# Kernel optimization log

Measured on AMD Instinct MI355X. Metric: run time of the kernel, lower is better.

## Reference

```python
import jax, jax.numpy as jnp
import numpy as np

B, S, D = 4, 2048, 512
H = 8
HD = D // H  # 64


def setup_inputs() -> dict:
    key = jax.random.key(0)
    k1, k2, k3 = jax.random.split(key, 3)
    x = jax.random.normal(k1, (B, S, D), dtype=jnp.float32)
    w_qkv = jax.random.normal(k2, (3 * D, D), dtype=jnp.float32) * (D ** -0.5)
    w_out = jax.random.normal(k3, (D, D), dtype=jnp.float32) * (D ** -0.5)
    return {"x": x, "w_qkv": w_qkv, "w_out": w_out}


def reference(x, w_qkv, w_out):
    b, s, d = x.shape
    # qkv projection (no bias), split into q,k,v
    qkv = jnp.einsum('bsd,ed->bse', x, w_qkv)  # [b, s, 3*d]
    q, k, v = jnp.split(qkv, 3, axis=2)
    # [b, s, h*hd] -> [b, h, s, hd]
    def to_heads(t):
        return t.reshape(b, s, H, HD).transpose(0, 2, 1, 3)
    q, k, v = to_heads(q), to_heads(k), to_heads(v)
    # NOTE: original module only scales by sqrt(head_dim) when mask is given;
    # with mask=None softmax is over raw QK^T scores.
    scores = jnp.einsum('bnid,bnjd->bnij', q, k)  # [b, h, s, s]
    attn = jax.nn.softmax(scores, axis=-1)
    o = jnp.einsum('bnij,bnjd->bnid', attn, v)  # [b, h, s, hd]
    o = o.transpose(0, 2, 1, 3).reshape(b, s, d)
    # dropout is identity (eval / drop_prob=0)
    return jnp.einsum('bsd,ed->bse', o, w_out)
```

## Files before the change

kernel.cpp:

```cpp
#include <hip/hip_runtime.h>
#include <hip/hip_bf16.h>

constexpr int B_  = 4;
constexpr int S_  = 2048;
constexpr int D_  = 512;
constexpr int H_  = 8;
constexpr int HD_ = 64;
constexpr int M_  = B_ * S_;

constexpr float LOG2E = 1.4426950408889634f;

typedef __attribute__((ext_vector_type(8))) short short8v;
typedef __attribute__((ext_vector_type(8))) _Float16 half8v;
typedef __attribute__((ext_vector_type(8))) unsigned short ushort8v;
typedef __attribute__((ext_vector_type(4))) float float4v;
typedef __attribute__((ext_vector_type(16))) float float16v;

__device__ __forceinline__ unsigned short f2bf(float x) {
    unsigned u = __builtin_bit_cast(unsigned, x);
    u += 0x7fffu + ((u >> 16) & 1u);
    return (unsigned short)(u >> 16);
}
__device__ __forceinline__ float bf2f(unsigned short h) {
    return __builtin_bit_cast(float, ((unsigned)h) << 16);
}
__device__ __forceinline__ unsigned short f2h(float x) {
    return __builtin_bit_cast(unsigned short, (_Float16)x);
}
__device__ __forceinline__ float fast_exp2(float x) {
#if __has_builtin(__builtin_amdgcn_exp2f)
    return __builtin_amdgcn_exp2f(x);
#else
    return exp2f(x);
#endif
}
__device__ __forceinline__ unsigned pack_bf16_trunc(float lo, float hi) {
    const unsigned ulo = __builtin_bit_cast(unsigned, lo);
    const unsigned uhi = __builtin_bit_cast(unsigned, hi);
#if __has_builtin(__builtin_amdgcn_perm)
    return __builtin_amdgcn_perm(uhi, ulo, 0x07060302u);
#else
    return (uhi & 0xffff0000u) | (ulo >> 16);
#endif
}
__device__ __forceinline__ void gload_lds16(const void* g, void* lds) {
    __builtin_amdgcn_global_load_lds((const __attribute__((address_space(1))) unsigned*)g,
                                     (__attribute__((address_space(3))) unsigned*)lds, 16, 0, 0);
}

__global__ __launch_bounds__(256) void prepass(const float* __restrict__ x,
                                               const float* __restrict__ wqkv,
                                               const float* __restrict__ wout,
                                               unsigned short* __restrict__ Xp,
                                               unsigned short* __restrict__ Wh,
                                               unsigned short* __restrict__ Wlq,
                                               unsigned short* __restrict__ Wob) {
    const int bid = blockIdx.x, t = threadIdx.x;
    if (bid < 2048) {
        const int flat = bid * 256 + t;
        const int m = flat >> 6, c = (flat & 63) * 8;
        const float4 a = *(const float4*)&x[(size_t)m * 512 + c];
        const float4 b = *(const float4*)&x[(size_t)m * 512 + c + 4];
        const float v[8] = {a.x, a.y, a.z, a.w, b.x, b.y, b.z, b.w};
        ushort8v hi, lo;
#pragma unroll
        for (int i = 0; i < 8; ++i) {
            const unsigned short h = f2bf(v[i]);
            hi[i] = h; lo[i] = f2bf(v[i] - bf2f(h));
        }
        *(ushort8v*)&Xp[(size_t)m * 1024 + c]       = hi;
        *(ushort8v*)&Xp[(size_t)m * 1024 + 512 + c] = lo;
    } else if (bid < 2048 + 384) {
        const int flat = (bid - 2048) * 256 + t;
        const int e = flat >> 6, c = (flat & 63) * 8;
        const float4 a = *(const float4*)&wqkv[(size_t)e * 512 + c];
        const float4 b = *(const float4*)&wqkv[(size_t)e * 512 + c + 4];
        const float v[8] = {a.x, a.y, a.z, a.w, b.x, b.y, b.z, b.w};
        ushort8v hi, lo;
#pragma unroll
        for (int i = 0; i < 8; ++i) {
            const unsigned short h = f2bf(v[i]);
            hi[i] = h; lo[i] = f2bf(v[i] - bf2f(h));
        }
        *(ushort8v*)&Wh[(size_t)e * 512 + c] = hi;
        if (e < 512) *(ushort8v*)&Wlq[(size_t)e * 512 + c] = lo;
    } else {
        const int flat = (bid - 2432) * 256 + t;
        const int e = flat >> 6, c = (flat & 63) * 8;
        const float4 a = *(const float4*)&wout[(size_t)e * 512 + c];
        const float4 b = *(const float4*)&wout[(size_t)e * 512 + c + 4];
        const float v[8] = {a.x, a.y, a.z, a.w, b.x, b.y, b.z, b.w};
        ushort8v hi;
#pragma unroll
        for (int i = 0; i < 8; ++i) hi[i] = f2bf(v[i]);
        *(ushort8v*)&Wob[(size_t)e * 512 + c] = hi;
    }
}

__global__ __launch_bounds__(256, 2) void gemm_qkv(const unsigned short* __restrict__ Xp,
                                                   const unsigned short* __restrict__ Wh,
                                                   const unsigned short* __restrict__ Wlq,
                                                   unsigned short* __restrict__ Qf,
                                                   unsigned short* __restrict__ KH,
                                                   unsigned short* __restrict__ VT) {
    __shared__ unsigned short Asm[2][128 * 64];
    __shared__ unsigned short Bsm[2][128 * 64];
    const int t = threadIdx.x, wv = t >> 6, lane = t & 63;
    const int fm = lane & 15, fq = lane >> 4;
    const int bid0 = blockIdx.x + 12 * blockIdx.y;
    const int xcd = bid0 & 7, ii = bid0 >> 3;
    const int x  = ii % 12;
    const int m0 = ((ii / 12) * 8 + xcd) * 128;
    const int slice = x >> 2;
    const int e0 = (x & 3) * 128;
    const bool vblk = (slice == 2);
    const int kiters = (slice == 0) ? 24 : 8;
    const int wrow = (wv >> 1) * 64, wcol = (wv & 1) * 64;

    const unsigned short* BbaseWh =
        Wh + (size_t)(e0 + (slice == 1 ? 512 : (slice == 2 ? 1024 : 0))) * 512;
    const unsigned short* BbaseWlq = Wlq + (size_t)e0 * 512;

    const int srow = t >> 3;
    const int skb0 = t & 7;

    float4v acc[4][4];
#pragma unroll
    for (int i = 0; i < 4; ++i)
#pragma unroll
        for (int j = 0; j < 4; ++j) acc[i][j] = (float4v){0.f, 0.f, 0.f, 0.f};

    {
#pragma unroll
        for (int i = 0; i < 4; ++i) {
            const int row = srow + 32 * i;
            const int kb = skb0 ^ (row & 7);
            gload_lds16(Xp + (size_t)(m0 + row) * 1024 + kb * 8,
                        &Asm[0][(wv * 64 + 256 * i) * 8]);
            gload_lds16(BbaseWh + (size_t)row * 512 + kb * 8,
                        &Bsm[0][(wv * 64 + 256 * i) * 8]);
        }
    }

    for (int kk = 0; kk < kiters; ++kk) {
        __syncthreads();

        if (kk + 1 < kiters) {
            const int nk = kk + 1;
            const int pass = nk >> 3;
            const int k0n = (nk & 7) * 64;
            const int nbuf = nk & 1;
            const int aoff = (slice == 0 && pass == 1) ? 512 : 0;
            const unsigned short* Bp = (slice == 0 && pass == 2) ? BbaseWlq : BbaseWh;
#pragma unroll
            for (int i = 0; i < 4; ++i) {
                const int row = srow + 32 * i;
                const int kb = skb0 ^ (row & 7);
                gload_lds16(Xp + (size_t)(m0 + row) * 1024 + aoff + k0n + kb * 8,
                            &Asm[nbuf][(wv * 64 + 256 * i) * 8]);
                gload_lds16(Bp + (size_t)row * 512 + k0n + kb * 8,
                            &Bsm[nbuf][(wv * 64 + 256 * i) * 8]);
            }
        }

        const int buf = kk & 1;
#pragma unroll
        for (int ks = 0; ks < 2; ++ks) {
            short8v af[4], bf[4];
#pragma unroll
            for (int mt = 0; mt < 4; ++mt) {
                const int row = wrow + mt * 16 + fm;
                af[mt] = *(const short8v*)&Asm[buf][row * 64 + 8 * ((4 * ks + fq) ^ (row & 7))];
            }
#pragma unroll
            for (int nt = 0; nt < 4; ++nt) {
                const int row = wcol + nt * 16 + fm;
                bf[nt] = *(const short8v*)&Bsm[buf][row * 64 + 8 * ((4 * ks + fq) ^ (row & 7))];
            }
            if (vblk) {
#pragma unroll
                for (int mt = 0; mt < 4; ++mt)
#pragma unroll
                    for (int nt = 0; nt < 4; ++nt)
                        acc[mt][nt] = __builtin_amdgcn_mfma_f32_16x16x32_bf16(bf[nt], af[mt], acc[mt][nt], 0, 0, 0);
            } else {
#pragma unroll
                for (int mt = 0; mt < 4; ++mt)
#pragma unroll
                    for (int nt = 0; nt < 4; ++nt)
                        acc[mt][nt] = __builtin_amdgcn_mfma_f32_16x16x32_bf16(af[mt], bf[nt], acc[mt][nt], 0, 0, 0);
            }
        }
    }

    if (!vblk) {
        unsigned short* __restrict__ dst = (slice == 0) ? Qf : KH;
        const float sc = (slice == 0) ? LOG2E : 1.0f;
#pragma unroll
        for (int mt = 0; mt < 4; ++mt)
#pragma unroll
            for (int nt = 0; nt < 4; ++nt) {
                const int e = e0 + wcol + nt * 16 + fm;
                const int h = e >> 6, hd = e & 63;
#pragma unroll
                for (int r = 0; r < 4; ++r) {
                    const int m = m0 + wrow + mt * 16 + 4 * fq + r;
                    const int b = m >> 11, s = m & 2047;
                    dst[((size_t)(b * 8 + h) * 2048 + s) * 64 + hd] =
                        f2h(acc[mt][nt][r] * sc);
                }
            }
    } else {
#pragma unroll
        for (int nt = 0; nt < 4; ++nt)
#pragma unroll
            for (int r = 0; r < 4; ++r) {
                const int e = e0 + wcol + nt * 16 + 4 * fq + r;
                const int h = e >> 6, hd = e & 63;
#pragma unroll
                for (int mt = 0; mt < 4; ++mt) {
                    const int m = m0 + wrow + mt * 16 + fm;
                    const int b = m >> 11, s = m & 2047;
                    const int s2 = (s & ~12) | ((s & 4) << 1) | ((s & 8) >> 1);
                    VT[((size_t)(b * 8 + h) * 64 + hd) * 2048 + s2] = f2bf(acc[mt][nt][r]);
                }
            }
    }
}

__global__ __launch_bounds__(256, 2) void attn(const unsigned short* __restrict__ Qfp,
                                               const unsigned short* __restrict__ KHp,
                                               const unsigned short* __restrict__ VTp,
                                               unsigned short* __restrict__ OB) {
    __shared__ unsigned short Ks[2][64 * 64];
    __shared__ unsigned short Vs[2][64 * 64];
    const int t = threadIdx.x, wv = t >> 6, lane = t & 63;
    const int lq = lane & 31;
    const int hf2 = lane >> 5;
    const int bid0 = blockIdx.x + 16 * blockIdx.y;
    const int xcd = bid0 & 7, ii = bid0 >> 3;
    const int bh = (ii & 3) * 8 + xcd;
    const int q0 = (ii >> 2) * 128;

    const unsigned short* qfp = Qfp + (size_t)bh * S_ * 64;
    const unsigned short* kh  = KHp + (size_t)bh * S_ * 64;
    const unsigned short* vt  = VTp + (size_t)bh * 64 * S_;

    const int srow = t >> 3;
    const int skb0 = t & 7;

#define STAGE_K(N, B) do {                                                      \
    _Pragma("unroll")                                                           \
    for (int i_ = 0; i_ < 2; ++i_) {                                            \
        const int row_ = srow + 32 * i_;                                        \
        const int kb_ = skb0 ^ (row_ & 7);                                      \
        gload_lds16(kh + (size_t)((N) * 64 + row_) * 64 + kb_ * 8,              \
                    &Ks[B][(wv * 64 + 256 * i_) * 8]);                          \
    } } while (0)

#define STAGE_V(N, B) do {                                                      \
    _Pragma("unroll")                                                           \
    for (int i_ = 0; i_ < 2; ++i_) {                                            \
        const int row_ = srow + 32 * i_;                                        \
        const int kb_ = skb0 ^ (row_ & 7);                                      \
        gload_lds16(vt + (size_t)row_ * S_ + (N) * 64 + kb_ * 8,                \
                    &Vs[B][(wv * 64 + 256 * i_) * 8]);                          \
    } } while (0)

#define QK_STEP(SN, KR) do {                                                    \
    _Pragma("unroll")                                                           \
    for (int jb_ = 0; jb_ < 2; ++jb_)                                           \
        _Pragma("unroll")                                                       \
        for (int r_ = 0; r_ < 16; ++r_) SN[jb_][r_] = 0.f;                      \
    _Pragma("unroll")                                                           \
    for (int kk_ = 0; kk_ < 4; ++kk_)                                           \
        _Pragma("unroll")                                                       \
        for (int jb_ = 0; jb_ < 2; ++jb_) {                                     \
            const int row_ = jb_ * 32 + lq;                                     \
            const int cb_ = 2 * kk_ + hf2;                                      \
            const half8v kf_ = *(const half8v*)&Ks[KR][row_ * 64 + 8 * (cb_ ^ (row_ & 7))]; \
            SN[jb_] = __builtin_amdgcn_mfma_f32_32x32x16_f16(kf_, qf[kk_], SN[jb_], 0, 0, 0); \
        } } while (0)

#define SOFTMAX_PV(SC, VR) do {                                                 \
    unsigned pk_[2][4][2];                                                      \
    _Pragma("unroll")                                                           \
    for (int jb_ = 0; jb_ < 2; ++jb_)                                           \
        _Pragma("unroll")                                                       \
        for (int g_ = 0; g_ < 4; ++g_) {                                        \
            const float p0_ = fast_exp2(SC[jb_][4 * g_ + 0]);                   \
            const float p1_ = fast_exp2(SC[jb_][4 * g_ + 1]);                   \
            const float p2_ = fast_exp2(SC[jb_][4 * g_ + 2]);                   \
            const float p3_ = fast_exp2(SC[jb_][4 * g_ + 3]);                   \
            lsum += (p0_ + p1_) + (p2_ + p3_);                                  \
            pk_[jb_][g_][0] = pack_bf16_trunc(p0_, p1_);                        \
            pk_[jb_][g_][1] = pack_bf16_trunc(p2_, p3_);                        \
        }                                                                       \
    __builtin_amdgcn_s_setprio(1);                                              \
    _Pragma("unroll")                                                           \
    for (int jc_ = 0; jc_ < 4; ++jc_) {                                         \
        const int jb_ = jc_ >> 1, gg_ = (jc_ & 1) * 2;                          \
        const uint4 uu_ = {pk_[jb_][gg_][0], pk_[jb_][gg_][1],                  \
                           pk_[jb_][gg_ + 1][0], pk_[jb_][gg_ + 1][1]};         \
        const short8v pa_ = __builtin_bit_cast(short8v, uu_);                   \
        _Pragma("unroll")                                                       \
        for (int db_ = 0; db_ < 2; ++db_) {                                     \
            const int vrow_ = db_ * 32 + lq;                                    \
            const int cb_ = 2 * jc_ + hf2;                                      \
            const short8v vf_ = *(const short8v*)&Vs[VR][vrow_ * 64 + 8 * (cb_ ^ (vrow_ & 7))]; \
            accO[db_] = __builtin_amdgcn_mfma_f32_32x32x16_bf16(pa_, vf_, accO[db_], 0, 0, 0);  \
        }                                                                       \
    }                                                                           \
    __builtin_amdgcn_s_setprio(0);                                              \
} while (0)

    STAGE_K(0, 0);
    STAGE_V(0, 0);
    STAGE_K(1, 1);

    half8v qf[4];
    {
        const int qrow = q0 + wv * 32 + lq;
#pragma unroll
        for (int kk = 0; kk < 4; ++kk)
            qf[kk] = *(const half8v*)&qfp[(size_t)qrow * 64 + kk * 16 + hf2 * 8];
    }

    float16v accO[2];
#pragma unroll
    for (int db = 0; db < 2; ++db)
#pragma unroll
        for (int r = 0; r < 16; ++r) accO[db][r] = 0.f;
    float lsum = 0.f;

    float16v sA[2], sB[2];

    __syncthreads();
    QK_STEP(sA, 0);
    __syncthreads();

    for (int jt = 0; jt < 32; jt += 2) {
        if (jt + 2 < 32) STAGE_K(jt + 2, 0);
        STAGE_V(jt + 1, 1);
        QK_STEP(sB, 1);
        SOFTMAX_PV(sA, 0);
        __syncthreads();
        if (jt + 3 < 32) STAGE_K(jt + 3, 1);
        if (jt + 2 < 32) {
            STAGE_V(jt + 2, 0);
            QK_STEP(sA, 0);
        }
        SOFTMAX_PV(sB, 1);
        __syncthreads();
    }

#undef STAGE_K
#undef STAGE_V
#undef QK_STEP
#undef SOFTMAX_PV

    const float ls = lsum + __shfl_xor(lsum, 32);
    const float invl = 1.f / ls;

    const int b = bh >> 3, hh = bh & 7;
#pragma unroll
    for (int g = 0; g < 4; ++g)
#pragma unroll
        for (int r = 0; r < 4; ++r) {
            const int qrow = r + 8 * g + 4 * hf2;
            const float inv = __shfl(invl, qrow);
            const int q = q0 + wv * 32 + qrow;
#pragma unroll
            for (int db = 0; db < 2; ++db)
                OB[((size_t)(b * 2048 + q)) * 512 + hh * 64 + db * 32 + lq] =
                    f2bf(accO[db][4 * g + r] * inv);
        }
}

__global__ __launch_bounds__(256) void gemm_out(const unsigned short* __restrict__ OB,
                                                const unsigned short* __restrict__ Wob,
                                                float* __restrict__ out) {
    __shared__ unsigned short Asm[2][128 * 64];
    __shared__ unsigned short Bsm[2][64 * 64];
    const int t = threadIdx.x, wv = t >> 6, lane = t & 63;
    const int fm = lane & 15, fq = lane >> 4;
    const int bid0 = blockIdx.x + 8 * blockIdx.y;
    const int xcd = bid0 & 7, ii = bid0 >> 3;
    const int e0 = (ii % 8) * 64;
    const int m0 = ((ii / 8) * 8 + xcd) * 128;
    const int wrow = (wv & 1) * 64, wcol = (wv >> 1) * 32;

    const int srow = t >> 3;
    const int skb0 = t & 7;

    float4v acc[4][2];
#pragma unroll
    for (int i = 0; i < 4; ++i)
#pragma unroll
        for (int j = 0; j < 2; ++j) acc[i][j] = (float4v){0.f, 0.f, 0.f, 0.f};

#pragma unroll
    for (int i = 0; i < 4; ++i) {
        const int row = srow + 32 * i;
        const int kb = skb0 ^ (row & 7);
        gload_lds16(OB + (size_t)(m0 + row) * 512 + kb * 8,
                    &Asm[0][(wv * 64 + 256 * i) * 8]);
    }
#pragma unroll
    for (int i = 0; i < 2; ++i) {
        const int row = srow + 32 * i;
        const int kb = skb0 ^ (row & 7);
        gload_lds16(Wob + (size_t)(e0 + row) * 512 + kb * 8,
                    &Bsm[0][(wv * 64 + 256 * i) * 8]);
    }

    for (int kk = 0; kk < 8; ++kk) {
        __syncthreads();
        if (kk + 1 < 8) {
            const int k0n = (kk + 1) * 64, nbuf = (kk + 1) & 1;
#pragma unroll
            for (int i = 0; i < 4; ++i) {
                const int row = srow + 32 * i;
                const int kb = skb0 ^ (row & 7);
                gload_lds16(OB + (size_t)(m0 + row) * 512 + k0n + kb * 8,
                            &Asm[nbuf][(wv * 64 + 256 * i) * 8]);
            }
#pragma unroll
            for (int i = 0; i < 2; ++i) {
                const int row = srow + 32 * i;
                const int kb = skb0 ^ (row & 7);
                gload_lds16(Wob + (size_t)(e0 + row) * 512 + k0n + kb * 8,
                            &Bsm[nbuf][(wv * 64 + 256 * i) * 8]);
            }
        }
        const int buf = kk & 1;
#pragma unroll
        for (int ks = 0; ks < 2; ++ks) {
            short8v af[4], bf[2];
#pragma unroll
            for (int mt = 0; mt < 4; ++mt) {
                const int row = wrow + mt * 16 + fm;
                af[mt] = *(const short8v*)&Asm[buf][row * 64 + 8 * ((4 * ks + fq) ^ (row & 7))];
            }
#pragma unroll
            for (int nt = 0; nt < 2; ++nt) {
                const int row = wcol + nt * 16 + fm;
                bf[nt] = *(const short8v*)&Bsm[buf][row * 64 + 8 * ((4 * ks + fq) ^ (row & 7))];
            }
#pragma unroll
            for (int mt = 0; mt < 4; ++mt)
#pragma unroll
                for (int nt = 0; nt < 2; ++nt)
                    acc[mt][nt] = __builtin_amdgcn_mfma_f32_16x16x32_bf16(af[mt], bf[nt], acc[mt][nt], 0, 0, 0);
        }
    }
#pragma unroll
    for (int mt = 0; mt < 4; ++mt)
#pragma unroll
        for (int nt = 0; nt < 2; ++nt)
#pragma unroll
            for (int r = 0; r < 4; ++r) {
                const int m = m0 + wrow + mt * 16 + 4 * fq + r;
                const int e = e0 + wcol + nt * 16 + fm;
                out[(size_t)m * 512 + e] = acc[mt][nt][r];
            }
}

extern "C" void kernel_launch(void* const* d_in, const int* in_sizes, int n_in,
                              void* d_out, int out_size, void* d_ws, size_t ws_size,
                              hipStream_t stream) {
    const float* x     = (const float*)d_in[0];
    const float* w_qkv = (const float*)d_in[1];
    const float* w_out = (const float*)d_in[2];
    float* out = (float*)d_out;

    char* p = (char*)d_ws;
    unsigned short* Xp  = (unsigned short*)p;  p += (size_t)M_ * 1024 * 2;
    unsigned short* Wh  = (unsigned short*)p;  p += (size_t)1536 * 512 * 2;
    unsigned short* Wlq = (unsigned short*)p;  p += (size_t)512 * 512 * 2;
    unsigned short* Wob = (unsigned short*)p;  p += (size_t)512 * 512 * 2;
    unsigned short* Qf  = (unsigned short*)p;  p += (size_t)32 * S_ * 64 * 2;
    unsigned short* KH  = (unsigned short*)p;  p += (size_t)32 * S_ * 64 * 2;
    unsigned short* VT  = (unsigned short*)p;  p += (size_t)32 * 64 * S_ * 2;
    unsigned short* OB  = Xp;

    prepass<<<2560, 256, 0, stream>>>(x, w_qkv, w_out, Xp, Wh, Wlq, Wob);
    gemm_qkv<<<dim3(12, 64), 256, 0, stream>>>(Xp, Wh, Wlq, Qf, KH, VT);
    attn<<<dim3(16, 32), 256, 0, stream>>>(Qf, KH, VT, OB);
    gemm_out<<<dim3(8, 64), 256, 0, stream>>>(OB, Wob, out);
}
```

Baseline: 161.1 us.

## Use single-pass fp16 QKV GEMM and enlarge output GEMM tiles

The QKV projection drops its split hi/lo bf16 scheme, where the Q slice ran three K passes. Inputs and weights are now converted once to fp16 and multiplied with f16 MFMA in a single pass, which cuts prepass writes and Q-slice GEMM work. The output GEMM moves from 128x64 to 128x128 tiles with 2-block occupancy to improve data reuse. The risk is lower Q precision feeding the unscaled softmax, and f2h must exist in the hidden helper lines.

```diff
diff --git a/kernel.cpp b/kernel.cpp
--- a/kernel.cpp
+++ b/kernel.cpp
@@ -51,9 +51,8 @@
 __global__ __launch_bounds__(256) void prepass(const float* __restrict__ x,
                                                const float* __restrict__ wqkv,
                                                const float* __restrict__ wout,
-                                               unsigned short* __restrict__ Xp,
-                                               unsigned short* __restrict__ Wh,
-                                               unsigned short* __restrict__ Wlq,
+                                               unsigned short* __restrict__ Xf,
+                                               unsigned short* __restrict__ Wf,
                                                unsigned short* __restrict__ Wob) {
     const int bid = blockIdx.x, t = threadIdx.x;
     if (bid < 2048) {
@@ -62,44 +61,35 @@
         const float4 a = *(const float4*)&x[(size_t)m * 512 + c];
         const float4 b = *(const float4*)&x[(size_t)m * 512 + c + 4];
         const float v[8] = {a.x, a.y, a.z, a.w, b.x, b.y, b.z, b.w};
-        ushort8v hi, lo;
-#pragma unroll
-        for (int i = 0; i < 8; ++i) {
-            const unsigned short h = f2bf(v[i]);
-            hi[i] = h; lo[i] = f2bf(v[i] - bf2f(h));
-        }
-        *(ushort8v*)&Xp[(size_t)m * 1024 + c]       = hi;
-        *(ushort8v*)&Xp[(size_t)m * 1024 + 512 + c] = lo;
+        ushort8v o;
+#pragma unroll
+        for (int i = 0; i < 8; ++i) o[i] = f2h(v[i]);
+        *(ushort8v*)&Xf[(size_t)m * 512 + c] = o;
     } else if (bid < 2048 + 384) {
         const int flat = (bid - 2048) * 256 + t;
         const int e = flat >> 6, c = (flat & 63) * 8;
         const float4 a = *(const float4*)&wqkv[(size_t)e * 512 + c];
         const float4 b = *(const float4*)&wqkv[(size_t)e * 512 + c + 4];
         const float v[8] = {a.x, a.y, a.z, a.w, b.x, b.y, b.z, b.w};
-        ushort8v hi, lo;
-#pragma unroll
-        for (int i = 0; i < 8; ++i) {
-            const unsigned short h = f2bf(v[i]);
-            hi[i] = h; lo[i] = f2bf(v[i] - bf2f(h));
-        }
-        *(ushort8v*)&Wh[(size_t)e * 512 + c] = hi;
-        if (e < 512) *(ushort8v*)&Wlq[(size_t)e * 512 + c] = lo;
+        ushort8v o;
+#pragma unroll
+        for (int i = 0; i < 8; ++i) o[i] = f2h(v[i]);
+        *(ushort8v*)&Wf[(size_t)e * 512 + c] = o;
     } else {
         const int flat = (bid - 2432) * 256 + t;
         const int e = flat >> 6, c = (flat & 63) * 8;
         const float4 a = *(const float4*)&wout[(size_t)e * 512 + c];
         const float4 b = *(const float4*)&wout[(size_t)e * 512 + c + 4];
         const float v[8] = {a.x, a.y, a.z, a.w, b.x, b.y, b.z, b.w};
-        ushort8v hi;
-#pragma unroll
-        for (int i = 0; i < 8; ++i) hi[i] = f2bf(v[i]);
-        *(ushort8v*)&Wob[(size_t)e * 512 + c] = hi;
-    }
-}
-
-__global__ __launch_bounds__(256, 2) void gemm_qkv(const unsigned short* __restrict__ Xp,
-                                                   const unsigned short* __restrict__ Wh,
-                                                   const unsigned short* __restrict__ Wlq,
+        ushort8v o;
+#pragma unroll
+        for (int i = 0; i < 8; ++i) o[i] = f2bf(v[i]);
+        *(ushort8v*)&Wob[(size_t)e * 512 + c] = o;
+    }
+}
+
+__global__ __launch_bounds__(256, 2) void gemm_qkv(const unsigned short* __restrict__ Xf,
+                                                   const unsigned short* __restrict__ Wf,
                                                    unsigned short* __restrict__ Qf,
                                                    unsigned short* __restrict__ KH,
                                                    unsigned short* __restrict__ VT) {
@@ -114,12 +104,9 @@
     const int slice = x >> 2;
     const int e0 = (x & 3) * 128;
     const bool vblk = (slice == 2);
-    const int kiters = (slice == 0) ? 24 : 8;
     const int wrow = (wv >> 1) * 64, wcol = (wv & 1) * 64;
 
-    const unsigned short* BbaseWh =
-        Wh + (size_t)(e0 + (slice == 1 ? 512 : (slice == 2 ? 1024 : 0))) * 512;
-    const unsigned short* BbaseWlq = Wlq + (size_t)e0 * 512;
+    const unsigned short* Bbase = Wf + (size_t)(e0 + slice * 512) * 512;
 
     const int srow = t >> 3;
     const int skb0 = t & 7;
@@ -130,35 +117,29 @@
 #pragma unroll
         for (int j = 0; j < 4; ++j) acc[i][j] = (float4v){0.f, 0.f, 0.f, 0.f};
 
-    {
-#pragma unroll
-        for (int i = 0; i < 4; ++i) {
-            const int row = srow + 32 * i;
-            const int kb = skb0 ^ (row & 7);
-            gload_lds16(Xp + (size_t)(m0 + row) * 1024 + kb * 8,
-                        &Asm[0][(wv * 64 + 256 * i) * 8]);
-            gload_lds16(BbaseWh + (size_t)row * 512 + kb * 8,
-                        &Bsm[0][(wv * 64 + 256 * i) * 8]);
-        }
-    }
-
-    for (int kk = 0; kk < kiters; ++kk) {
+#pragma unroll
+    for (int i = 0; i < 4; ++i) {
+        const int row = srow + 32 * i;
+        const int kb = skb0 ^ (row & 7);
+        gload_lds16(Xf + (size_t)(m0 + row) * 512 + kb * 8,
+                    &Asm[0][(wv * 64 + 256 * i) * 8]);
+        gload_lds16(Bbase + (size_t)row * 512 + kb * 8,
+                    &Bsm[0][(wv * 64 + 256 * i) * 8]);
+    }
+
+    for (int kk = 0; kk < 8; ++kk) {
         __syncthreads();
 
-        if (kk + 1 < kiters) {
-            const int nk = kk + 1;
-            const int pass = nk >> 3;
-            const int k0n = (nk & 7) * 64;
-            const int nbuf = nk & 1;
-            const int aoff = (slice == 0 && pass == 1) ? 512 : 0;
-            const unsigned short* Bp = (slice == 0 && pass == 2) ? BbaseWlq : BbaseWh;
+        if (kk + 1 < 8) {
+            const int k0n = (kk + 1) * 64;
+            const int nbuf = (kk + 1) & 1;
 #pragma unroll
             for (int i = 0; i < 4; ++i) {
                 const int row = srow + 32 * i;
                 const int kb = skb0 ^ (row & 7);
-                gload_lds16(Xp + (size_t)(m0 + row) * 1024 + aoff + k0n + kb * 8,
+                gload_lds16(Xf + (size_t)(m0 + row) * 512 + k0n + kb * 8,
                             &Asm[nbuf][(wv * 64 + 256 * i) * 8]);
-                gload_lds16(Bp + (size_t)row * 512 + k0n + kb * 8,
+                gload_lds16(Bbase + (size_t)row * 512 + k0n + kb * 8,
                             &Bsm[nbuf][(wv * 64 + 256 * i) * 8]);
             }
         }
@@ -166,29 +147,29 @@
         const int buf = kk & 1;
 #pragma unroll
         for (int ks = 0; ks < 2; ++ks) {
-            short8v af[4], bf[4];
+            half8v af[4], bf[4];
 #pragma unroll
             for (int mt = 0; mt < 4; ++mt) {
                 const int row = wrow + mt * 16 + fm;
-                af[mt] = *(const short8v*)&Asm[buf][row * 64 + 8 * ((4 * ks + fq) ^ (row & 7))];
+                af[mt] = *(const half8v*)&Asm[buf][row * 64 + 8 * ((4 * ks + fq) ^ (row & 7))];
             }
 #pragma unroll
             for (int nt = 0; nt < 4; ++nt) {
                 const int row = wcol + nt * 16 + fm;
-                bf[nt] = *(const short8v*)&Bsm[buf][row * 64 + 8 * ((4 * ks + fq) ^ (row & 7))];
+                bf[nt] = *(const half8v*)&Bsm[buf][row * 64 + 8 * ((4 * ks + fq) ^ (row & 7))];
             }
             if (vblk) {
 #pragma unroll
                 for (int mt = 0; mt < 4; ++mt)
 #pragma unroll
                     for (int nt = 0; nt < 4; ++nt)
-                        acc[mt][nt] = __builtin_amdgcn_mfma_f32_16x16x32_bf16(bf[nt], af[mt], acc[mt][nt], 0, 0, 0);
+                        acc[mt][nt] = __builtin_amdgcn_mfma_f32_16x16x32_f16(bf[nt], af[mt], acc[mt][nt], 0, 0, 0);
             } else {
 #pragma unroll
                 for (int mt = 0; mt < 4; ++mt)
 #pragma unroll
                     for (int nt = 0; nt < 4; ++nt)
-                        acc[mt][nt] = __builtin_amdgcn_mfma_f32_16x16x32_bf16(af[mt], bf[nt], acc[mt][nt], 0, 0, 0);
+                        acc[mt][nt] = __builtin_amdgcn_mfma_f32_16x16x32_f16(af[mt], bf[nt], acc[mt][nt], 0, 0, 0);
             }
         }
     }
@@ -377,27 +358,27 @@
         }
 }
 
-__global__ __launch_bounds__(256) void gemm_out(const unsigned short* __restrict__ OB,
-                                                const unsigned short* __restrict__ Wob,
-                                                float* __restrict__ out) {
+__global__ __launch_bounds__(256, 2) void gemm_out(const unsigned short* __restrict__ OB,
+                                                   const unsigned short* __restrict__ Wob,
+                                                   float* __restrict__ out) {
     __shared__ unsigned short Asm[2][128 * 64];
-    __shared__ unsigned short Bsm[2][64 * 64];
+    __shared__ unsigned short Bsm[2][128 * 64];
     const int t = threadIdx.x, wv = t >> 6, lane = t & 63;
     const int fm = lane & 15, fq = lane >> 4;
-    const int bid0 = blockIdx.x + 8 * blockIdx.y;
+    const int bid0 = blockIdx.x + 4 * blockIdx.y;
     const int xcd = bid0 & 7, ii = bid0 >> 3;
-    const int e0 = (ii % 8) * 64;
-    const int m0 = ((ii / 8) * 8 + xcd) * 128;
-    const int wrow = (wv & 1) * 64, wcol = (wv >> 1) * 32;
+    const int e0 = (ii % 4) * 128;
+    const int m0 = ((ii / 4) * 8 + xcd) * 128;
+    const int wrow = (wv >> 1) * 64, wcol = (wv & 1) * 64;
 
     const int srow = t >> 3;
     const int skb0 = t & 7;
 
-    float4v acc[4][2];
+    float4v acc[4][4];
 #pragma unroll
     for (int i = 0; i < 4; ++i)
 #pragma unroll
-        for (int j = 0; j < 2; ++j) acc[i][j] = (float4v){0.f, 0.f, 0.f, 0.f};
+        for (int j = 0; j < 4; ++j) acc[i][j] = (float4v){0.f, 0.f, 0.f, 0.f};
 
 #pragma unroll
     for (int i = 0; i < 4; ++i) {
@@ -405,11 +386,6 @@
         const int kb = skb0 ^ (row & 7);
         gload_lds16(OB + (size_t)(m0 + row) * 512 + kb * 8,
                     &Asm[0][(wv * 64 + 256 * i) * 8]);
-    }
-#pragma unroll
-    for (int i = 0; i < 2; ++i) {
-        const int row = srow + 32 * i;
-        const int kb = skb0 ^ (row & 7);
         gload_lds16(Wob + (size_t)(e0 + row) * 512 + kb * 8,
                     &Bsm[0][(wv * 64 + 256 * i) * 8]);
     }
@@ -424,11 +400,6 @@
                 const int kb = skb0 ^ (row & 7);
                 gload_lds16(OB + (size_t)(m0 + row) * 512 + k0n + kb * 8,
                             &Asm[nbuf][(wv * 64 + 256 * i) * 8]);
-            }
-#pragma unroll
-            for (int i = 0; i < 2; ++i) {
-                const int row = srow + 32 * i;
-                const int kb = skb0 ^ (row & 7);
                 gload_lds16(Wob + (size_t)(e0 + row) * 512 + k0n + kb * 8,
                             &Bsm[nbuf][(wv * 64 + 256 * i) * 8]);
             }
@@ -436,28 +407,28 @@
         const int buf = kk & 1;
 #pragma unroll
         for (int ks = 0; ks < 2; ++ks) {
-            short8v af[4], bf[2];
+            short8v af[4], bf[4];
 #pragma unroll
             for (int mt = 0; mt < 4; ++mt) {
                 const int row = wrow + mt * 16 + fm;
                 af[mt] = *(const short8v*)&Asm[buf][row * 64 + 8 * ((4 * ks + fq) ^ (row & 7))];
             }
 #pragma unroll
-            for (int nt = 0; nt < 2; ++nt) {
+            for (int nt = 0; nt < 4; ++nt) {
                 const int row = wcol + nt * 16 + fm;
                 bf[nt] = *(const short8v*)&Bsm[buf][row * 64 + 8 * ((4 * ks + fq) ^ (row & 7))];
             }
 #pragma unroll
             for (int mt = 0; mt < 4; ++mt)
 #pragma unroll
-                for (int nt = 0; nt < 2; ++nt)
+                for (int nt = 0; nt < 4; ++nt)
                     acc[mt][nt] = __builtin_amdgcn_mfma_f32_16x16x32_bf16(af[mt], bf[nt], acc[mt][nt], 0, 0, 0);
         }
     }
 #pragma unroll
     for (int mt = 0; mt < 4; ++mt)
 #pragma unroll
-        for (int nt = 0; nt < 2; ++nt)
+        for (int nt = 0; nt < 4; ++nt)
 #pragma unroll
             for (int r = 0; r < 4; ++r) {
                 const int m = m0 + wrow + mt * 16 + 4 * fq + r;
@@ -475,17 +446,16 @@
     float* out = (float*)d_out;
 
     char* p = (char*)d_ws;
-    unsigned short* Xp  = (unsigned short*)p;  p += (size_t)M_ * 1024 * 2;
-    unsigned short* Wh  = (unsigned short*)p;  p += (size_t)1536 * 512 * 2;
-    unsigned short* Wlq = (unsigned short*)p;  p += (size_t)512 * 512 * 2;
+    unsigned short* Xf  = (unsigned short*)p;  p += (size_t)M_ * 512 * 2;
+    unsigned short* Wf  = (unsigned short*)p;  p += (size_t)1536 * 512 * 2;
     unsigned short* Wob = (unsigned short*)p;  p += (size_t)512 * 512 * 2;
     unsigned short* Qf  = (unsigned short*)p;  p += (size_t)32 * S_ * 64 * 2;
     unsigned short* KH  = (unsigned short*)p;  p += (size_t)32 * S_ * 64 * 2;
     unsigned short* VT  = (unsigned short*)p;  p += (size_t)32 * 64 * S_ * 2;
-    unsigned short* OB  = Xp;
-
-    prepass<<<2560, 256, 0, stream>>>(x, w_qkv, w_out, Xp, Wh, Wlq, Wob);
-    gemm_qkv<<<dim3(12, 64), 256, 0, stream>>>(Xp, Wh, Wlq, Qf, KH, VT);
+    unsigned short* OB  = Xf;
+
+    prepass<<<2560, 256, 0, stream>>>(x, w_qkv, w_out, Xf, Wf, Wob);
+    gemm_qkv<<<dim3(12, 64), 256, 0, stream>>>(Xf, Wf, Qf, KH, VT);
     attn<<<dim3(16, 32), 256, 0, stream>>>(Qf, KH, VT, OB);
-    gemm_out<<<dim3(8, 64), 256, 0, stream>>>(OB, Wob, out);
-}
+    gemm_out<<<dim3(4, 64), 256, 0, stream>>>(OB, Wob, out);
+}
```

After: 140.9 us. 12.6% less time.
